# Performance work log

Measured on AMD Instinct MI355X. Metric: run time of the kernel, lower is better.

The kernel has to match this reference:

```python
import jax, jax.numpy as jnp
import numpy as np

B, T, H, W, VD, AD, HD, QD = 256, 10, 7, 7, 512, 128, 256, 128  # QD = 512//latent_dim(4)
BETA = 0.5

def _lin(k, out_d, in_d):
    kw, kb = jax.random.split(k)
    s = 1.0 / np.sqrt(in_d)
    return (jax.random.uniform(kw, (out_d, in_d), jnp.float32, -s, s),
            jax.random.uniform(kb, (out_d,), jnp.float32, -s, s))

def setup_inputs() -> dict:
    key = jax.random.key(0)
    ks = jax.random.split(key, 20)
    d = {}
    d['video'] = jax.random.normal(ks[0], (B, T, H, W, VD), jnp.float32)
    d['audio'] = jax.random.normal(ks[1], (T, B, AD), jnp.float32)
    d['wq'], d['bq'] = _lin(ks[2], QD, VD)
    d['wk'], d['bk'] = _lin(ks[3], QD, VD)
    d['wv'], d['bv'] = _lin(ks[4], VD, VD)
    d['ln_g'] = jnp.ones((VD,), jnp.float32)
    d['ln_b'] = jnp.zeros((VD,), jnp.float32)
    d['w_ave'], d['b_ave'] = _lin(ks[5], HD, VD)
    d['w_v3'], d['b_v3'] = _lin(ks[6], HD, VD)
    d['w_avatt'], d['b_avatt'] = _lin(ks[7], 1, HD)
    d['w_a1'], d['b_a1'] = _lin(ks[8], VD, AD)
    d['w_v1'], d['b_v1'] = _lin(ks[9], VD, VD)
    d['w_bn'], d['b_bn'] = _lin(ks[10], HD, VD)
    d['w_ca'], d['b_ca'] = _lin(ks[11], VD, HD)
    d['w_v2'], d['b_v2'] = _lin(ks[12], HD, VD)
    d['w_a2'], d['b_a2'] = _lin(ks[13], HD, AD)
    d['w_sa'], d['b_sa'] = _lin(ks[14], 1, HD)
    return d

def linear(x, w, b):
    return jnp.matmul(x, w.T) + b

def layer_norm(x, g, b, eps=1e-5):
    mu = jnp.mean(x, -1, keepdims=True)
    var = jnp.mean(jnp.square(x - mu), -1, keepdims=True)
    return (x - mu) * jax.lax.rsqrt(var + eps) * g + b

def reference(video, audio, wq, bq, wk, bk, wv, bv, ln_g, ln_b,
              w_ave, b_ave, w_v3, b_v3, w_avatt, b_avatt,
              w_a1, b_a1, w_v1, b_v1, w_bn, b_bn, w_ca, b_ca,
              w_v2, b_v2, w_a2, b_a2, w_sa, b_sa):
    relu = jax.nn.relu
    audio_bt = jnp.transpose(audio, (1, 0, 2))            # [B,T,AD]
    raw_audio_feature = audio_bt
    audio_feature = audio_bt.reshape(B * T, AD)
    vf = video.reshape(B, T, H * W, VD)                   # [B,T,49,VD]
    raw_visual_feature = vf
    # --- visual self-attention (single head, latent_dim=4) ---
    q = linear(vf, wq, bq).reshape(B * T, H * W, QD)
    k = linear(vf, wk, bk).reshape(B * T, H * W, QD)
    v = linear(vf, wv, bv).reshape(B * T, H * W, VD)
    attn = jax.nn.softmax(jnp.einsum('bnd,bmd->bnm', q, k), axis=-1)
    out = jnp.einsum('bnm,bmd->bnd', attn, v)
    vf2 = layer_norm(vf.reshape(B * T, H * W, VD) + out, ln_g, ln_b)  # dropout in eval mode
    # --- self spatial attention branch ---
    video_avg = relu(linear(vf2.sum(1) / (H * W), w_ave, b_ave))[:, None, :]  # [B*T,1,HD]
    self_q = relu(linear(vf2, w_v3, b_v3)) * video_avg                        # [B*T,49,HD]
    self_maps = jax.nn.softmax(
        jnp.tanh(linear(self_q, w_avatt, b_avatt)).transpose(0, 2, 1), axis=-1)  # [B*T,1,49]
    self_att_feat = jnp.einsum('bon,bnd->bod', self_maps, vf2).reshape(B, T, VD)
    # --- audio-guided channel attention ---
    aq1 = relu(linear(audio_feature, w_a1, b_a1))[:, None, :]                 # [B*T,1,VD]
    vq1 = relu(linear(vf2, w_v1, b_v1))                                       # [B*T,49,VD]
    avq = relu(linear((aq1 * vq1).mean(-2), w_bn, b_bn))                      # [B*T,HD]
    ch_maps = jax.nn.sigmoid(linear(avq, w_ca, b_ca)).reshape(B, T, 1, VD)
    c_att = (raw_visual_feature * (ch_maps + 1.0)).reshape(B * T, H * W, VD)
    # --- audio-guided spatial attention ---
    cq = relu(linear(c_att, w_v2, b_v2))                                      # [B*T,49,HD]
    aq2 = relu(linear(audio_feature, w_a2, b_a2))[:, None, :]                 # [B*T,1,HD]
    sp_maps = jax.nn.softmax(
        jnp.tanh(linear(cq * aq2, w_sa, b_sa)).transpose(0, 2, 1), axis=-1)   # [B*T,1,49]
    c_s = jnp.einsum('bon,bnd->bod', sp_maps, c_att).reshape(B, T, VD)
    c_s = c_s + BETA * jax.nn.sigmoid(self_att_feat) * c_s
    return (c_s, raw_audio_feature)
```

## Files before the change

### kernel.cpp

```cpp
#include <hip/hip_runtime.h>

#define B_   256
#define T_   10
#define BT   2560
#define NSP  49
#define VD   512
#define AD   128
#define HD   256
#define QD   128
#define BETA 0.5f

typedef __bf16 bf16_t;
typedef bf16_t bf16x8 __attribute__((ext_vector_type(8)));
typedef float  f32x4  __attribute__((ext_vector_type(4)));

#define GLDS(g, l) __builtin_amdgcn_global_load_lds(                          \
    (const __attribute__((address_space(1))) void*)(g),                       \
    (__attribute__((address_space(3))) void*)(l), 16, 0, 0)

__global__ __launch_bounds__(128) void k_audio(const float* __restrict__ audio,
                                               float* __restrict__ out2) {
  int bt = blockIdx.x;
  int b = bt / T_, t = bt - b * T_;
  out2[(size_t)bt * AD + threadIdx.x] = audio[((size_t)t * B_ + b) * AD + threadIdx.x];
}

__global__ __launch_bounds__(256) void k_split(const float* __restrict__ x,
                                               bf16_t* __restrict__ hi,
                                               bf16_t* __restrict__ lo) {
  const size_t i8 = (size_t)blockIdx.x * 256 + threadIdx.x;
  const float4 x0 = ((const float4*)x)[2 * i8];
  const float4 x1 = ((const float4*)x)[2 * i8 + 1];
  const float xs[8] = {x0.x, x0.y, x0.z, x0.w, x1.x, x1.y, x1.z, x1.w};
  bf16x8 h, l;
#pragma unroll
  for (int j = 0; j < 8; ++j) {
    const bf16_t hb = (bf16_t)xs[j];
    h[j] = hb;
    l[j] = (bf16_t)(xs[j] - (float)hb);
  }
  ((bf16x8*)hi)[i8] = h;
  ((bf16x8*)lo)[i8] = l;
}

__device__ __forceinline__ bf16x8 ldsread(const unsigned char* plane, int rblk, int lane) {
  const int row = (rblk << 4) + (lane & 15);
  const int chunk = (lane >> 4) ^ ((row >> 1) & 3);
  return *(const bf16x8*)(plane + row * 64 + chunk * 16);
}

template <int ACT>
__global__ __launch_bounds__(256, 2) void k_mgemm(
    const bf16_t* __restrict__ Ahi, const bf16_t* __restrict__ Alo,
    const bf16_t* __restrict__ Whi, const bf16_t* __restrict__ Wlo,
    const float* __restrict__ bias, float* __restrict__ C,
    int M, int N, int K) {
  __shared__ __align__(16) unsigned char smem[2][4][8192];
  const int t = threadIdx.x;
  const int lane = t & 63, wid = t >> 6;
  const int wr = wid >> 1, wc = wid & 1;
  const int rowBase = blockIdx.y * 128;
  const int colBase = blockIdx.x * 128;

  f32x4 acc[4][4] = {};

  const bf16_t* srcs[4] = {Ahi, Alo, Whi, Wlo};
  const int rb[4] = {rowBase, rowBase, colBase, colBase};

  auto stage = [&](int buf, int kt) {
    const int k0 = kt << 5;
#pragma unroll
    for (int p = 0; p < 4; ++p) {
#pragma unroll
      for (int issue = 0; issue < 2; ++issue) {
        const int orow = issue * 64 + wid * 16 + (lane >> 2);
        const int sc = (lane & 3) ^ ((orow >> 1) & 3);
        const bf16_t* g = srcs[p] + (size_t)(rb[p] + orow) * K + k0 + sc * 8;
        unsigned char* l = &smem[buf][p][issue * 4096 + wid * 1024];
        GLDS(g, l);
      }
    }
  };

  const int NK = K >> 5;
  stage(0, 0);
  for (int kt = 0; kt < NK; ++kt) {
    const int cur = kt & 1;
    __syncthreads();
    if (kt + 1 < NK) stage(cur ^ 1, kt + 1);
    const unsigned char* pa_hi = smem[cur][0];
    const unsigned char* pa_lo = smem[cur][1];
    const unsigned char* pw_hi = smem[cur][2];
    const unsigned char* pw_lo = smem[cur][3];
    bf16x8 ah[4], al[4], bh[4], bl[4];
#pragma unroll
    for (int m = 0; m < 4; ++m) {
      ah[m] = ldsread(pa_hi, wr * 4 + m, lane);
      al[m] = ldsread(pa_lo, wr * 4 + m, lane);
    }
#pragma unroll
    for (int n = 0; n < 4; ++n) {
      bh[n] = ldsread(pw_hi, wc * 4 + n, lane);
      bl[n] = ldsread(pw_lo, wc * 4 + n, lane);
    }
#pragma unroll
    for (int m = 0; m < 4; ++m)
#pragma unroll
      for (int n = 0; n < 4; ++n) {
        acc[m][n] = __builtin_amdgcn_mfma_f32_16x16x32_bf16(ah[m], bh[n], acc[m][n], 0, 0, 0);
        acc[m][n] = __builtin_amdgcn_mfma_f32_16x16x32_bf16(ah[m], bl[n], acc[m][n], 0, 0, 0);
        acc[m][n] = __builtin_amdgcn_mfma_f32_16x16x32_bf16(al[m], bh[n], acc[m][n], 0, 0, 0);
      }
  }

  const int r4 = lane >> 4;
  const int cn = lane & 15;
#pragma unroll
  for (int n = 0; n < 4; ++n) {
    const int col = colBase + wc * 64 + n * 16 + cn;
    const float bb = bias[col];
#pragma unroll
    for (int m = 0; m < 4; ++m) {
      const int row0 = rowBase + wr * 64 + m * 16 + r4 * 4;
#pragma unroll
      for (int r = 0; r < 4; ++r) {
        float x = acc[m][n][r] + bb;
        if (ACT == 1) x = fmaxf(x, 0.f);
        C[(size_t)(row0 + r) * N + col] = x;
      }
    }
  }
}

template <int ACT>
__global__ __launch_bounds__(256) void k_gemm(const float* __restrict__ A,
                                              const float* __restrict__ W,
                                              const float* __restrict__ bias,
                                              float* __restrict__ C,
                                              int M, int N, int K, float alpha) {
  __shared__ __align__(16) float As[8][132];
  __shared__ __align__(16) float Ws[8][132];
  const int t = threadIdx.x;
  const int tx = t & 15, ty = t >> 4;
  const int rowBase = blockIdx.y * 128;
  const int colBase = blockIdx.x * 128;
  const int lrow = t >> 1, lq = t & 1;
  const float* Ap = A + (size_t)(rowBase + lrow) * K + lq * 4;
  const float* Wp = W + (size_t)(colBase + lrow) * K + lq * 4;
  float acc[8][8] = {};
  for (int k0 = 0; k0 < K; k0 += 8) {
    const float4 av = *(const float4*)(Ap + k0);
    const float4 wv = *(const float4*)(Wp + k0);
    __syncthreads();
    As[lq * 4 + 0][lrow] = av.x; As[lq * 4 + 1][lrow] = av.y;
    As[lq * 4 + 2][lrow] = av.z; As[lq * 4 + 3][lrow] = av.w;
    Ws[lq * 4 + 0][lrow] = wv.x; Ws[lq * 4 + 1][lrow] = wv.y;
    Ws[lq * 4 + 2][lrow] = wv.z; Ws[lq * 4 + 3][lrow] = wv.w;
    __syncthreads();
#pragma unroll
    for (int kk = 0; kk < 8; ++kk) {
      const float4 a0 = *(const float4*)&As[kk][ty * 8];
      const float4 a1 = *(const float4*)&As[kk][ty * 8 + 4];
      const float4 w0 = *(const float4*)&Ws[kk][tx * 8];
      const float4 w1 = *(const float4*)&Ws[kk][tx * 8 + 4];
      const float a_[8] = {a0.x, a0.y, a0.z, a0.w, a1.x, a1.y, a1.z, a1.w};
      const float w_[8] = {w0.x, w0.y, w0.z, w0.w, w1.x, w1.y, w1.z, w1.w};
#pragma unroll
      for (int i = 0; i < 8; ++i)
#pragma unroll
        for (int j = 0; j < 8; ++j)
          acc[i][j] = fmaf(a_[i], w_[j], acc[i][j]);
    }
  }
  const float4 b0 = *(const float4*)(bias + colBase + tx * 8);
  const float4 b1 = *(const float4*)(bias + colBase + tx * 8 + 4);
  const float bb[8] = {b0.x, b0.y, b0.z, b0.w, b1.x, b1.y, b1.z, b1.w};
#pragma unroll
  for (int i = 0; i < 8; ++i) {
    float* crow = C + (size_t)(rowBase + ty * 8 + i) * N + colBase + tx * 8;
    float o[8];
#pragma unroll
    for (int j = 0; j < 8; ++j) {
      float x = acc[i][j] * alpha + bb[j];
      if (ACT == 1) x = fmaxf(x, 0.f);
      if (ACT == 2) x = 1.f / (1.f + __expf(-x));
      o[j] = x;
    }
    *(float4*)(crow)     = make_float4(o[0], o[1], o[2], o[3]);
    *(float4*)(crow + 4) = make_float4(o[4], o[5], o[6], o[7]);
  }
}

__global__ __launch_bounds__(512) void k_attn(const float* __restrict__ q,
                                              const float* __restrict__ k,
                                              const float* __restrict__ v,
                                              const float* __restrict__ vf,
                                              const float* __restrict__ ln_g,
                                              const float* __restrict__ ln_b,
                                              bf16_t* __restrict__ vf2hi,
                                              bf16_t* __restrict__ vf2lo,
                                              float* __restrict__ vsum) {
  const int bt = blockIdx.x;
  const int t = threadIdx.x;
  __shared__ float qs[NSP][129];
  __shared__ float ks[NSP][129];
  __shared__ float at[NSP][50];
  __shared__ float red[2][NSP][8];
  __shared__ float mu_s[NSP], rs_s[NSP];

  const float* qg = q + (size_t)bt * NSP * QD;
  const float* kg = k + (size_t)bt * NSP * QD;
  for (int i = t; i < NSP * QD; i += 512) {
    int n = i >> 7, c = i & (QD - 1);
    qs[n][c] = qg[i];
    ks[n][c] = kg[i];
  }
  __syncthreads();
  for (int p = t; p < NSP * NSP; p += 512) {
    int n = p / NSP, m = p - n * NSP;
    float s = 0.f;
#pragma unroll 16
    for (int j = 0; j < QD; ++j) s = fmaf(qs[n][j], ks[m][j], s);
    at[n][m] = s;
  }
  __syncthreads();
  if (t < NSP) {
    float mx = -1e30f;
    for (int m2 = 0; m2 < NSP; ++m2) mx = fmaxf(mx, at[t][m2]);
    float sum = 0.f;
    for (int m2 = 0; m2 < NSP; ++m2) { float e = __expf(at[t][m2] - mx); at[t][m2] = e; sum += e; }
    float inv = 1.f / sum;
    for (int m2 = 0; m2 < NSP; ++m2) at[t][m2] *= inv;
  }
  __syncthreads();
  const int d = t;
  const float* vg  = v  + (size_t)bt * NSP * VD + d;
  const float* vfg = vf + (size_t)bt * NSP * VD + d;
  float xv[NSP] = {};
  for (int m2 = 0; m2 < NSP; ++m2) {
    const float vm = vg[(size_t)m2 * VD];
#pragma unroll
    for (int n = 0; n < NSP; ++n) xv[n] = fmaf(at[n][m2], vm, xv[n]);
  }
#pragma unroll
  for (int n = 0; n < NSP; ++n) xv[n] += vfg[(size_t)n * VD];
  const int lane = t & 63, wid = t >> 6;
#pragma unroll
  for (int n = 0; n < NSP; ++n) {
    float s1 = xv[n], s2 = xv[n] * xv[n];
    for (int off = 32; off; off >>= 1) { s1 += __shfl_down(s1, off); s2 += __shfl_down(s2, off); }
    if (lane == 0) { red[0][n][wid] = s1; red[1][n][wid] = s2; }
  }
  __syncthreads();
  if (t < NSP) {
    float s1 = 0.f, s2 = 0.f;
    for (int w2 = 0; w2 < 8; ++w2) { s1 += red[0][t][w2]; s2 += red[1][t][w2]; }
    const float mu = s1 * (1.f / VD);
    const float var = s2 * (1.f / VD) - mu * mu;
    mu_s[t] = mu;
    rs_s[t] = rsqrtf(var + 1e-5f);
  }
  __syncthreads();
  const float gd = ln_g[d], bd = ln_b[d];
  bf16_t* oh = vf2hi + (size_t)bt * NSP * VD + d;
  bf16_t* ol = vf2lo + (size_t)bt * NSP * VD + d;
  float vs = 0.f;
#pragma unroll
  for (int n = 0; n < NSP; ++n) {
    const float y = (xv[n] - mu_s[n]) * rs_s[n] * gd + bd;
    const bf16_t hb = (bf16_t)y;
    oh[(size_t)n * VD] = hb;
    ol[(size_t)n * VD] = (bf16_t)(y - (float)hb);
    vs += y;
  }
  vsum[(size_t)bt * VD + d] = vs;
}

__global__ __launch_bounds__(256) void k_score_einsum(
    const float* __restrict__ Cm, const float* __restrict__ gate,
    const float* __restrict__ wvv, const float* __restrict__ bsc,
    const bf16_t* __restrict__ Vhi, const bf16_t* __restrict__ Vlo,
    const float* __restrict__ saf_in, float* __restrict__ outp) {
  const int bt = blockIdx.x, t = threadIdx.x;
  __shared__ float us[HD];
  __shared__ float sc[NSP];
  __shared__ float mp[NSP + 1];
  us[t] = gate[(size_t)bt * HD + t] * wvv[t];
  __syncthreads();
  const int lane = t & 63, w = t >> 6;
  const float bias0 = bsc[0];
  for (int n = w; n < NSP; n += 4) {
    const float* row = Cm + ((size_t)bt * NSP + n) * HD;
    float s = 0.f;
#pragma unroll
    for (int i = 0; i < HD / 64; ++i) s = fmaf(row[lane + 64 * i], us[lane + 64 * i], s);
    for (int off = 32; off; off >>= 1) s += __shfl_down(s, off);
    if (lane == 0) sc[n] = tanhf(s + bias0);
  }
  __syncthreads();
  if (t == 0) {
    float mx = -1e30f;
    for (int n = 0; n < NSP; ++n) mx = fmaxf(mx, sc[n]);
    float sum = 0.f;
    for (int n = 0; n < NSP; ++n) { float e = __expf(sc[n] - mx); mp[n] = e; sum += e; }
    float inv = 1.f / sum;
    for (int n = 0; n < NSP; ++n) mp[n] *= inv;
  }
  __syncthreads();
  for (int d = t; d < VD; d += 256) {
    const bf16_t* vh = Vhi + (size_t)bt * NSP * VD + d;
    const bf16_t* vl = Vlo + (size_t)bt * NSP * VD + d;
    float a = 0.f;
#pragma unroll
    for (int n = 0; n < NSP; ++n) {
      const float vv = (float)vh[(size_t)n * VD] + (float)vl[(size_t)n * VD];
      a = fmaf(mp[n], vv, a);
    }
    if (saf_in) {
      const float sg = 1.f / (1.f + __expf(-saf_in[(size_t)bt * VD + d]));
      a *= (1.f + BETA * sg);
    }
    outp[(size_t)bt * VD + d] = a;
  }
}

__global__ __launch_bounds__(512) void k_vq1mean(const float* __restrict__ vq1,
                                                 const float* __restrict__ aq1,
                                                 float* __restrict__ tmean) {
  const int bt = blockIdx.x, d = threadIdx.x;
  const float* p = vq1 + (size_t)bt * NSP * VD + d;
  float s = 0.f;
#pragma unroll
  for (int n = 0; n < NSP; ++n) s += p[(size_t)n * VD];
  tmean[(size_t)bt * VD + d] = s * (1.f / 49.f) * aq1[(size_t)bt * VD + d];
}

__global__ __launch_bounds__(256) void k_catt(const float* __restrict__ video,
                                              const float* __restrict__ ch,
                                              bf16_t* __restrict__ hi,
                                              bf16_t* __restrict__ lo) {
  const size_t i8 = (size_t)blockIdx.x * 256 + threadIdx.x;
  const size_t i = i8 * 8;
  const size_t bt = i / ((size_t)NSP * VD);
  const int d = (int)(i & (VD - 1));
  const float4 v0 = ((const float4*)(video + i))[0];
  const float4 v1 = ((const float4*)(video + i))[1];
  const float4 c0 = *(const float4*)(ch + bt * VD + d);
  const float4 c1 = *(const float4*)(ch + bt * VD + d + 4);
  const float xs[8] = {v0.x * (c0.x + 1.f), v0.y * (c0.y + 1.f),
                       v0.z * (c0.z + 1.f), v0.w * (c0.w + 1.f),
                       v1.x * (c1.x + 1.f), v1.y * (c1.y + 1.f),
                       v1.z * (c1.z + 1.f), v1.w * (c1.w + 1.f)};
  bf16x8 h, l;
#pragma unroll
  for (int j = 0; j < 8; ++j) {
    const bf16_t hb = (bf16_t)xs[j];
    h[j] = hb;
    l[j] = (bf16_t)(xs[j] - (float)hb);
  }
  ((bf16x8*)hi)[i8] = h;
  ((bf16x8*)lo)[i8] = l;
}

extern "C" void kernel_launch(void* const* d_in, const int* in_sizes, int n_in,
                              void* d_out, int out_size, void* d_ws, size_t ws_size,
                              hipStream_t stream) {
  const float* video  = (const float*)d_in[0];
  const float* audio  = (const float*)d_in[1];
  const float* wq     = (const float*)d_in[2];  const float* bq     = (const float*)d_in[3];
  const float* wk     = (const float*)d_in[4];  const float* bk     = (const float*)d_in[5];
  const float* wv     = (const float*)d_in[6];  const float* bv     = (const float*)d_in[7];
  const float* ln_g   = (const float*)d_in[8];  const float* ln_b   = (const float*)d_in[9];
  const float* w_ave  = (const float*)d_in[10]; const float* b_ave  = (const float*)d_in[11];
  const float* w_v3   = (const float*)d_in[12]; const float* b_v3   = (const float*)d_in[13];
  const float* w_avatt= (const float*)d_in[14]; const float* b_avatt= (const float*)d_in[15];
  const float* w_a1   = (const float*)d_in[16]; const float* b_a1   = (const float*)d_in[17];
  const float* w_v1   = (const float*)d_in[18]; const float* b_v1   = (const float*)d_in[19];
  const float* w_bn   = (const float*)d_in[20]; const float* b_bn   = (const float*)d_in[21];
  const float* w_ca   = (const float*)d_in[22]; const float* b_ca   = (const float*)d_in[23];
  const float* w_v2   = (const float*)d_in[24]; const float* b_v2   = (const float*)d_in[25];
  const float* w_a2   = (const float*)d_in[26]; const float* b_a2   = (const float*)d_in[27];
  const float* w_sa   = (const float*)d_in[28]; const float* b_sa   = (const float*)d_in[29];

  float* out = (float*)d_out;
  float* out_audio = out + (size_t)BT * VD;

  const size_t M = (size_t)BT * NSP;

  unsigned char* p = (unsigned char*)d_ws;
  auto carve = [&](size_t bytes) { unsigned char* r = p; p += (bytes + 255) & ~(size_t)255; return r; };
  bf16_t* vhi = (bf16_t*)carve(M * VD * 2);
  bf16_t* vlo = (bf16_t*)carve(M * VD * 2);
  bf16_t* wqh = (bf16_t*)carve((size_t)QD * VD * 2);
  bf16_t* wql = (bf16_t*)carve((size_t)QD * VD * 2);
  bf16_t* wkh = (bf16_t*)carve((size_t)QD * VD * 2);
  bf16_t* wkl = (bf16_t*)carve((size_t)QD * VD * 2);
  bf16_t* wvh = (bf16_t*)carve((size_t)VD * VD * 2);
  bf16_t* wvl = (bf16_t*)carve((size_t)VD * VD * 2);
  bf16_t* w3h = (bf16_t*)carve((size_t)HD * VD * 2);
  bf16_t* w3l = (bf16_t*)carve((size_t)HD * VD * 2);
  bf16_t* w1h = (bf16_t*)carve((size_t)VD * VD * 2);
  bf16_t* w1l = (bf16_t*)carve((size_t)VD * VD * 2);
  bf16_t* w2h = (bf16_t*)carve((size_t)HD * VD * 2);
  bf16_t* w2l = (bf16_t*)carve((size_t)HD * VD * 2);
  float* q_   = (float*)carve(M * QD * 4);
  float* k_   = (float*)carve(M * QD * 4);
  float* v_   = (float*)carve(M * VD * 4);
  float* vsum = (float*)carve((size_t)BT * VD * 4);
  float* vavg = (float*)carve((size_t)BT * HD * 4);
  float* aq1  = (float*)carve((size_t)BT * VD * 4);
  float* aq2  = (float*)carve((size_t)BT * HD * 4);
  float* tmean= (float*)carve((size_t)BT * VD * 4);
  float* avq  = (float*)carve((size_t)BT * HD * 4);
  float* saf  = (float*)carve((size_t)BT * VD * 4);
  float* ch   = (float*)carve((size_t)BT * VD * 4);
  float* C1   = q_;
  float* vq1  = v_;
  float* C2   = q_;
  bf16_t *vf2hi = vhi, *vf2lo = vlo, *catthi = vhi, *cattlo = vlo;

  const dim3 blk(256);

  k_audio<<<BT, AD, 0, stream>>>(audio, out_audio);

  k_split<<<(int)(M * VD / 8 / 256), blk, 0, stream>>>(video, vhi, vlo);
  k_split<<<QD * VD / 8 / 256, blk, 0, stream>>>(wq, wqh, wql);
  k_split<<<QD * VD / 8 / 256, blk, 0, stream>>>(wk, wkh, wkl);
  k_split<<<VD * VD / 8 / 256, blk, 0, stream>>>(wv, wvh, wvl);
  k_split<<<HD * VD / 8 / 256, blk, 0, stream>>>(w_v3, w3h, w3l);
  k_split<<<VD * VD / 8 / 256, blk, 0, stream>>>(w_v1, w1h, w1l);
  k_split<<<HD * VD / 8 / 256, blk, 0, stream>>>(w_v2, w2h, w2l);

  k_mgemm<0><<<dim3(QD / 128, M / 128), blk, 0, stream>>>(vhi, vlo, wqh, wql, bq, q_, M, QD, VD);
  k_mgemm<0><<<dim3(QD / 128, M / 128), blk, 0, stream>>>(vhi, vlo, wkh, wkl, bk, k_, M, QD, VD);
  k_mgemm<0><<<dim3(VD / 128, M / 128), blk, 0, stream>>>(vhi, vlo, wvh, wvl, bv, v_, M, VD, VD);
  k_attn<<<BT, 512, 0, stream>>>(q_, k_, v_, video, ln_g, ln_b, vf2hi, vf2lo, vsum);

  k_gemm<1><<<dim3(HD / 128, BT / 128), blk, 0, stream>>>(vsum, w_ave, b_ave, vavg, BT, HD, VD, 1.f / 49.f);
  k_gemm<1><<<dim3(VD / 128, BT / 128), blk, 0, stream>>>(out_audio, w_a1, b_a1, aq1, BT, VD, AD, 1.f);
  k_gemm<1><<<dim3(HD / 128, BT / 128), blk, 0, stream>>>(out_audio, w_a2, b_a2, aq2, BT, HD, AD, 1.f);

  k_mgemm<1><<<dim3(HD / 128, M / 128), blk, 0, stream>>>(vf2hi, vf2lo, w3h, w3l, b_v3, C1, M, HD, VD);
  k_score_einsum<<<BT, 256, 0, stream>>>(C1, vavg, w_avatt, b_avatt, vf2hi, vf2lo, nullptr, saf);

  k_mgemm<1><<<dim3(VD / 128, M / 128), blk, 0, stream>>>(vf2hi, vf2lo, w1h, w1l, b_v1, vq1, M, VD, VD);
  k_vq1mean<<<BT, VD, 0, stream>>>(vq1, aq1, tmean);
  k_gemm<1><<<dim3(HD / 128, BT / 128), blk, 0, stream>>>(tmean, w_bn, b_bn, avq, BT, HD, VD, 1.f);
  k_gemm<2><<<dim3(VD / 128, BT / 128), blk, 0, stream>>>(avq, w_ca, b_ca, ch, BT, VD, HD, 1.f);
  k_catt<<<(int)(M * VD / 8 / 256), blk, 0, stream>>>(video, ch, catthi, cattlo);

  k_mgemm<1><<<dim3(HD / 128, M / 128), blk, 0, stream>>>(catthi, cattlo, w2h, w2l, b_v2, C2, M, HD, VD);
  k_score_einsum<<<BT, 256, 0, stream>>>(C2, aq2, w_sa, b_sa, catthi, cattlo, saf, out);
}
```

Measured before the change: 2.397 ms.

## Fuse QKV projections into one bf16-split GEMM and MFMA-based attention kernel

```diff
diff --git a/kernel.cpp b/kernel.cpp
--- a/kernel.cpp
+++ b/kernel.cpp
@@ -17,12 +17,23 @@
 #define GLDS(g, l) __builtin_amdgcn_global_load_lds(                          \
     (const __attribute__((address_space(1))) void*)(g),                       \
     (__attribute__((address_space(3))) void*)(l), 16, 0, 0)
+#define MFMA16(a, b, c) __builtin_amdgcn_mfma_f32_16x16x32_bf16(a, b, c, 0, 0, 0)
 
 __global__ __launch_bounds__(128) void k_audio(const float* __restrict__ audio,
                                                float* __restrict__ out2) {
   int bt = blockIdx.x;
   int b = bt / T_, t = bt - b * T_;
   out2[(size_t)bt * AD + threadIdx.x] = audio[((size_t)t * B_ + b) * AD + threadIdx.x];
+}
+
+__global__ __launch_bounds__(256) void k_bcat(const float* __restrict__ bq,
+                                              const float* __restrict__ bk,
+                                              const float* __restrict__ bv,
+                                              float* __restrict__ bcat) {
+  int t = blockIdx.x * 256 + threadIdx.x;
+  if (t < 128) bcat[t] = bq[t];
+  else if (t < 256) bcat[t] = bk[t - 128];
+  else if (t < 768) bcat[t] = bv[t - 256];
 }
 
 __global__ __launch_bounds__(256) void k_split(const float* __restrict__ x,
@@ -49,11 +60,12 @@
   return *(const bf16x8*)(plane + row * 64 + chunk * 16);
 }
 
-template <int ACT>
+template <int ACT, int OUT>
 __global__ __launch_bounds__(256, 2) void k_mgemm(
     const bf16_t* __restrict__ Ahi, const bf16_t* __restrict__ Alo,
     const bf16_t* __restrict__ Whi, const bf16_t* __restrict__ Wlo,
     const float* __restrict__ bias, float* __restrict__ C,
+    bf16_t* __restrict__ Chi, bf16_t* __restrict__ Clo,
     int M, int N, int K) {
   __shared__ __align__(16) unsigned char smem[2][4][8192];
   const int t = threadIdx.x;
@@ -107,9 +119,9 @@
     for (int m = 0; m < 4; ++m)
 #pragma unroll
       for (int n = 0; n < 4; ++n) {
-        acc[m][n] = __builtin_amdgcn_mfma_f32_16x16x32_bf16(ah[m], bh[n], acc[m][n], 0, 0, 0);
-        acc[m][n] = __builtin_amdgcn_mfma_f32_16x16x32_bf16(ah[m], bl[n], acc[m][n], 0, 0, 0);
-        acc[m][n] = __builtin_amdgcn_mfma_f32_16x16x32_bf16(al[m], bh[n], acc[m][n], 0, 0, 0);
+        acc[m][n] = MFMA16(ah[m], bh[n], acc[m][n]);
+        acc[m][n] = MFMA16(ah[m], bl[n], acc[m][n]);
+        acc[m][n] = MFMA16(al[m], bh[n], acc[m][n]);
       }
   }
 
@@ -126,9 +138,205 @@
       for (int r = 0; r < 4; ++r) {
         float x = acc[m][n][r] + bb;
         if (ACT == 1) x = fmaxf(x, 0.f);
-        C[(size_t)(row0 + r) * N + col] = x;
-      }
-    }
+        const size_t idx = (size_t)(row0 + r) * N + col;
+        if (OUT == 0) {
+          C[idx] = x;
+        } else {
+          const bf16_t hb = (bf16_t)x;
+          Chi[idx] = hb;
+          Clo[idx] = (bf16_t)(x - (float)hb);
+        }
+      }
+    }
+  }
+}
+
+__global__ __launch_bounds__(512, 4) void k_attn2(
+    const bf16_t* __restrict__ ohi, const bf16_t* __restrict__ olo,
+    const float* __restrict__ vf, const float* __restrict__ ln_g,
+    const float* __restrict__ ln_b, bf16_t* __restrict__ vf2hi,
+    bf16_t* __restrict__ vf2lo, float* __restrict__ vsum) {
+  const int bt = blockIdx.x;
+  const int t = threadIdx.x;
+  const int lane = t & 63, w = t >> 6;
+  const int g = lane >> 4, li = lane & 15;
+  const int r = w & 3, h = w >> 2;
+  const size_t rowbase = (size_t)bt * NSP;
+
+  __shared__ __align__(16) unsigned char smem[69632];
+  __shared__ float red[2][2][4][16];
+  __shared__ float lnred[2][2][4][16];
+  __shared__ float vs_lds[4][512];
+
+  for (int u = t; u < 4096; u += 512) {
+    const int pl = u >> 10, row = (u >> 4) & 63, c = u & 15;
+    const bf16_t* src = (pl & 1) ? olo : ohi;
+    bf16x8 val = *(const bf16x8*)(src + (rowbase + row) * 768 + (pl >> 1) * 128 + c * 8);
+    *(bf16x8*)(smem + pl * 17408 + row * 272 + c * 16) = val;
+  }
+  __syncthreads();
+
+  f32x4 sacc[2] = {};
+#pragma unroll
+  for (int ks = 0; ks < 4; ++ks) {
+    const bf16x8 ah = *(const bf16x8*)(smem + 0 * 17408 + (r * 16 + li) * 272 + ks * 64 + g * 16);
+    const bf16x8 al = *(const bf16x8*)(smem + 1 * 17408 + (r * 16 + li) * 272 + ks * 64 + g * 16);
+#pragma unroll
+    for (int ct = 0; ct < 2; ++ct) {
+      const int m = (h * 2 + ct) * 16 + li;
+      const bf16x8 bh = *(const bf16x8*)(smem + 2 * 17408 + m * 272 + ks * 64 + g * 16);
+      const bf16x8 bl = *(const bf16x8*)(smem + 3 * 17408 + m * 272 + ks * 64 + g * 16);
+      sacc[ct] = MFMA16(ah, bh, sacc[ct]);
+      sacc[ct] = MFMA16(ah, bl, sacc[ct]);
+      sacc[ct] = MFMA16(al, bh, sacc[ct]);
+    }
+  }
+
+  const int m0 = (h * 2 + 0) * 16 + li;
+  const int m1 = (h * 2 + 1) * 16 + li;
+  float e0[4], e1[4];
+#pragma unroll
+  for (int reg = 0; reg < 4; ++reg) {
+    float s0 = (m0 < NSP) ? sacc[0][reg] : -1e30f;
+    float s1 = (m1 < NSP) ? sacc[1][reg] : -1e30f;
+    float mx = fmaxf(s0, s1);
+#pragma unroll
+    for (int off = 1; off < 16; off <<= 1) mx = fmaxf(mx, __shfl_xor(mx, off));
+    if (li == 0) red[0][h][r][g * 4 + reg] = mx;
+  }
+  __syncthreads();
+#pragma unroll
+  for (int reg = 0; reg < 4; ++reg) {
+    const float mx = fmaxf(red[0][0][r][g * 4 + reg], red[0][1][r][g * 4 + reg]);
+    e0[reg] = (m0 < NSP) ? __expf(sacc[0][reg] - mx) : 0.f;
+    e1[reg] = (m1 < NSP) ? __expf(sacc[1][reg] - mx) : 0.f;
+    float su = e0[reg] + e1[reg];
+#pragma unroll
+    for (int off = 1; off < 16; off <<= 1) su += __shfl_xor(su, off);
+    if (li == 0) red[1][h][r][g * 4 + reg] = su;
+  }
+  __syncthreads();
+#pragma unroll
+  for (int reg = 0; reg < 4; ++reg) {
+    const float inv = 1.f / (red[1][0][r][g * 4 + reg] + red[1][1][r][g * 4 + reg]);
+    const int nrow = r * 16 + g * 4 + reg;
+#pragma unroll
+    for (int ct = 0; ct < 2; ++ct) {
+      const int m = (h * 2 + ct) * 16 + li;
+      const float pv = (ct ? e1[reg] : e0[reg]) * inv;
+      const bf16_t ph = (bf16_t)pv;
+      *(bf16_t*)(smem + 0 * 9216 + nrow * 144 + m * 2) = ph;
+      *(bf16_t*)(smem + 1 * 9216 + nrow * 144 + m * 2) = (bf16_t)(pv - (float)ph);
+    }
+  }
+  __syncthreads();
+
+  bf16x8 pa[2][2];
+#pragma unroll
+  for (int ks = 0; ks < 2; ++ks)
+#pragma unroll
+    for (int pl = 0; pl < 2; ++pl)
+      pa[ks][pl] = *(const bf16x8*)(smem + pl * 9216 + (r * 16 + li) * 144 + ks * 64 + g * 16);
+
+  f32x4 oacc[4][4] = {};
+  for (int c = 0; c < 4; ++c) {
+    if (c > 0) __syncthreads();
+    for (int u = t; u < 1024; u += 512) {
+      const int pl = u >> 9, mc = (u >> 6) & 7, dp = u & 63;
+      const bf16_t* src = pl ? olo : ohi;
+      const bf16_t* base = src + (rowbase + mc * 8) * 768 + 256 + c * 128 + dp * 2;
+      bf16x8 r0, r1;
+#pragma unroll
+      for (int j = 0; j < 8; ++j) {
+        const ushort2 vv = *(const ushort2*)(base + (size_t)j * 768);
+        r0[j] = __builtin_bit_cast(bf16_t, (unsigned short)vv.x);
+        r1[j] = __builtin_bit_cast(bf16_t, (unsigned short)vv.y);
+      }
+      unsigned char* vt = smem + 18432 + pl * 18432;
+      *(bf16x8*)(vt + (dp * 2 + 0) * 144 + mc * 16) = r0;
+      *(bf16x8*)(vt + (dp * 2 + 1) * 144 + mc * 16) = r1;
+    }
+    __syncthreads();
+#pragma unroll
+    for (int qd = 0; qd < 4; ++qd) {
+      const int drow = (h * 4 + qd) * 16 + li;
+#pragma unroll
+      for (int ks = 0; ks < 2; ++ks) {
+        const bf16x8 bh = *(const bf16x8*)(smem + 18432 + 0 * 18432 + drow * 144 + ks * 64 + g * 16);
+        const bf16x8 bl = *(const bf16x8*)(smem + 18432 + 1 * 18432 + drow * 144 + ks * 64 + g * 16);
+        oacc[c][qd] = MFMA16(pa[ks][0], bh, oacc[c][qd]);
+        oacc[c][qd] = MFMA16(pa[ks][0], bl, oacc[c][qd]);
+        oacc[c][qd] = MFMA16(pa[ks][1], bh, oacc[c][qd]);
+      }
+    }
+  }
+
+#pragma unroll
+  for (int c = 0; c < 4; ++c)
+#pragma unroll
+    for (int qd = 0; qd < 4; ++qd) {
+      const int d = c * 128 + (h * 4 + qd) * 16 + li;
+#pragma unroll
+      for (int reg = 0; reg < 4; ++reg) {
+        const int n = r * 16 + g * 4 + reg;
+        if (n < NSP) oacc[c][qd][reg] += vf[(rowbase + n) * 512 + d];
+      }
+    }
+  float mu[4], rs[4];
+#pragma unroll
+  for (int reg = 0; reg < 4; ++reg) {
+    float s1 = 0.f, s2 = 0.f;
+#pragma unroll
+    for (int c = 0; c < 4; ++c)
+#pragma unroll
+      for (int qd = 0; qd < 4; ++qd) {
+        const float x = oacc[c][qd][reg];
+        s1 += x; s2 += x * x;
+      }
+#pragma unroll
+    for (int off = 1; off < 16; off <<= 1) {
+      s1 += __shfl_xor(s1, off);
+      s2 += __shfl_xor(s2, off);
+    }
+    if (li == 0) { lnred[0][h][r][g * 4 + reg] = s1; lnred[1][h][r][g * 4 + reg] = s2; }
+  }
+  __syncthreads();
+#pragma unroll
+  for (int reg = 0; reg < 4; ++reg) {
+    const float s1 = lnred[0][0][r][g * 4 + reg] + lnred[0][1][r][g * 4 + reg];
+    const float s2 = lnred[1][0][r][g * 4 + reg] + lnred[1][1][r][g * 4 + reg];
+    const float m_ = s1 * (1.f / VD);
+    mu[reg] = m_;
+    rs[reg] = rsqrtf(s2 * (1.f / VD) - m_ * m_ + 1e-5f);
+  }
+
+#pragma unroll
+  for (int c = 0; c < 4; ++c)
+#pragma unroll
+    for (int qd = 0; qd < 4; ++qd) {
+      const int d = c * 128 + (h * 4 + qd) * 16 + li;
+      const float gd = ln_g[d], bd = ln_b[d];
+      float vp = 0.f;
+#pragma unroll
+      for (int reg = 0; reg < 4; ++reg) {
+        const int n = r * 16 + g * 4 + reg;
+        const float y = (oacc[c][qd][reg] - mu[reg]) * rs[reg] * gd + bd;
+        if (n < NSP) {
+          const size_t idx = (rowbase + n) * 512 + d;
+          const bf16_t hb = (bf16_t)y;
+          vf2hi[idx] = hb;
+          vf2lo[idx] = (bf16_t)(y - (float)hb);
+          vp += y;
+        }
+      }
+#pragma unroll
+      for (int off = 16; off < 64; off <<= 1) vp += __shfl_xor(vp, off);
+      if (g == 0) vs_lds[r][d] = vp;
+    }
+  __syncthreads();
+  if (t < 512) {
+    const float s = vs_lds[0][t] + vs_lds[1][t] + vs_lds[2][t] + vs_lds[3][t];
+    vsum[(size_t)bt * 512 + t] = s;
   }
 }
 
@@ -191,91 +399,6 @@
   }
 }
 
-__global__ __launch_bounds__(512) void k_attn(const float* __restrict__ q,
-                                              const float* __restrict__ k,
-                                              const float* __restrict__ v,
-                                              const float* __restrict__ vf,
-                                              const float* __restrict__ ln_g,
-                                              const float* __restrict__ ln_b,
-                                              bf16_t* __restrict__ vf2hi,
-                                              bf16_t* __restrict__ vf2lo,
-                                              float* __restrict__ vsum) {
-  const int bt = blockIdx.x;
-  const int t = threadIdx.x;
-  __shared__ float qs[NSP][129];
-  __shared__ float ks[NSP][129];
-  __shared__ float at[NSP][50];
-  __shared__ float red[2][NSP][8];
-  __shared__ float mu_s[NSP], rs_s[NSP];
-
-  const float* qg = q + (size_t)bt * NSP * QD;
-  const float* kg = k + (size_t)bt * NSP * QD;
-  for (int i = t; i < NSP * QD; i += 512) {
-    int n = i >> 7, c = i & (QD - 1);
-    qs[n][c] = qg[i];
-    ks[n][c] = kg[i];
-  }
-  __syncthreads();
-  for (int p = t; p < NSP * NSP; p += 512) {
-    int n = p / NSP, m = p - n * NSP;
-    float s = 0.f;
-#pragma unroll 16
-    for (int j = 0; j < QD; ++j) s = fmaf(qs[n][j], ks[m][j], s);
-    at[n][m] = s;
-  }
-  __syncthreads();
-  if (t < NSP) {
-    float mx = -1e30f;
-    for (int m2 = 0; m2 < NSP; ++m2) mx = fmaxf(mx, at[t][m2]);
-    float sum = 0.f;
-    for (int m2 = 0; m2 < NSP; ++m2) { float e = __expf(at[t][m2] - mx); at[t][m2] = e; sum += e; }
-    float inv = 1.f / sum;
-    for (int m2 = 0; m2 < NSP; ++m2) at[t][m2] *= inv;
-  }
-  __syncthreads();
-  const int d = t;
-  const float* vg  = v  + (size_t)bt * NSP * VD + d;
-  const float* vfg = vf + (size_t)bt * NSP * VD + d;
-  float xv[NSP] = {};
-  for (int m2 = 0; m2 < NSP; ++m2) {
-    const float vm = vg[(size_t)m2 * VD];
-#pragma unroll
-    for (int n = 0; n < NSP; ++n) xv[n] = fmaf(at[n][m2], vm, xv[n]);
-  }
-#pragma unroll
-  for (int n = 0; n < NSP; ++n) xv[n] += vfg[(size_t)n * VD];
-  const int lane = t & 63, wid = t >> 6;
-#pragma unroll
-  for (int n = 0; n < NSP; ++n) {
-    float s1 = xv[n], s2 = xv[n] * xv[n];
-    for (int off = 32; off; off >>= 1) { s1 += __shfl_down(s1, off); s2 += __shfl_down(s2, off); }
-    if (lane == 0) { red[0][n][wid] = s1; red[1][n][wid] = s2; }
-  }
-  __syncthreads();
-  if (t < NSP) {
-    float s1 = 0.f, s2 = 0.f;
-    for (int w2 = 0; w2 < 8; ++w2) { s1 += red[0][t][w2]; s2 += red[1][t][w2]; }
-    const float mu = s1 * (1.f / VD);
-    const float var = s2 * (1.f / VD) - mu * mu;
-    mu_s[t] = mu;
-    rs_s[t] = rsqrtf(var + 1e-5f);
-  }
-  __syncthreads();
-  const float gd = ln_g[d], bd = ln_b[d];
-  bf16_t* oh = vf2hi + (size_t)bt * NSP * VD + d;
-  bf16_t* ol = vf2lo + (size_t)bt * NSP * VD + d;
-  float vs = 0.f;
-#pragma unroll
-  for (int n = 0; n < NSP; ++n) {
-    const float y = (xv[n] - mu_s[n]) * rs_s[n] * gd + bd;
-    const bf16_t hb = (bf16_t)y;
-    oh[(size_t)n * VD] = hb;
-    ol[(size_t)n * VD] = (bf16_t)(y - (float)hb);
-    vs += y;
-  }
-  vsum[(size_t)bt * VD + d] = vs;
-}
-
 __global__ __launch_bounds__(256) void k_score_einsum(
     const float* __restrict__ Cm, const float* __restrict__ gate,
     const float* __restrict__ wvv, const float* __restrict__ bsc,
@@ -386,69 +509,70 @@
   float* out_audio = out + (size_t)BT * VD;
 
   const size_t M = (size_t)BT * NSP;
+  const size_t Mpad = M + 64;
 
   unsigned char* p = (unsigned char*)d_ws;
   auto carve = [&](size_t bytes) { unsigned char* r = p; p += (bytes + 255) & ~(size_t)255; return r; };
-  bf16_t* vhi = (bf16_t*)carve(M * VD * 2);
-  bf16_t* vlo = (bf16_t*)carve(M * VD * 2);
-  bf16_t* wqh = (bf16_t*)carve((size_t)QD * VD * 2);
-  bf16_t* wql = (bf16_t*)carve((size_t)QD * VD * 2);
-  bf16_t* wkh = (bf16_t*)carve((size_t)QD * VD * 2);
-  bf16_t* wkl = (bf16_t*)carve((size_t)QD * VD * 2);
-  bf16_t* wvh = (bf16_t*)carve((size_t)VD * VD * 2);
-  bf16_t* wvl = (bf16_t*)carve((size_t)VD * VD * 2);
-  bf16_t* w3h = (bf16_t*)carve((size_t)HD * VD * 2);
-  bf16_t* w3l = (bf16_t*)carve((size_t)HD * VD * 2);
-  bf16_t* w1h = (bf16_t*)carve((size_t)VD * VD * 2);
-  bf16_t* w1l = (bf16_t*)carve((size_t)VD * VD * 2);
-  bf16_t* w2h = (bf16_t*)carve((size_t)HD * VD * 2);
-  bf16_t* w2l = (bf16_t*)carve((size_t)HD * VD * 2);
-  float* q_   = (float*)carve(M * QD * 4);
-  float* k_   = (float*)carve(M * QD * 4);
-  float* v_   = (float*)carve(M * VD * 4);
-  float* vsum = (float*)carve((size_t)BT * VD * 4);
-  float* vavg = (float*)carve((size_t)BT * HD * 4);
-  float* aq1  = (float*)carve((size_t)BT * VD * 4);
-  float* aq2  = (float*)carve((size_t)BT * HD * 4);
-  float* tmean= (float*)carve((size_t)BT * VD * 4);
-  float* avq  = (float*)carve((size_t)BT * HD * 4);
-  float* saf  = (float*)carve((size_t)BT * VD * 4);
-  float* ch   = (float*)carve((size_t)BT * VD * 4);
-  float* C1   = q_;
-  float* vq1  = v_;
-  float* C2   = q_;
-  bf16_t *vf2hi = vhi, *vf2lo = vlo, *catthi = vhi, *cattlo = vlo;
+  bf16_t* vhi  = (bf16_t*)carve(M * VD * 2);
+  bf16_t* vlo  = (bf16_t*)carve(M * VD * 2);
+  bf16_t* wch  = (bf16_t*)carve((size_t)768 * VD * 2);
+  bf16_t* wcl  = (bf16_t*)carve((size_t)768 * VD * 2);
+  bf16_t* w3h  = (bf16_t*)carve((size_t)HD * VD * 2);
+  bf16_t* w3l  = (bf16_t*)carve((size_t)HD * VD * 2);
+  bf16_t* w1h  = (bf16_t*)carve((size_t)VD * VD * 2);
+  bf16_t* w1l  = (bf16_t*)carve((size_t)VD * VD * 2);
+  bf16_t* w2h  = (bf16_t*)carve((size_t)HD * VD * 2);
+  bf16_t* w2l  = (bf16_t*)carve((size_t)HD * VD * 2);
+  float*  bcat = (float*)carve(768 * 4);
+  bf16_t* o_hi = (bf16_t*)carve(Mpad * 768 * 2 * 2);
+  bf16_t* o_lo = o_hi + Mpad * 768;
+  float* vsum  = (float*)carve((size_t)BT * VD * 4);
+  float* vavg  = (float*)carve((size_t)BT * HD * 4);
+  float* aq1   = (float*)carve((size_t)BT * VD * 4);
+  float* aq2   = (float*)carve((size_t)BT * HD * 4);
+  float* tmean = (float*)carve((size_t)BT * VD * 4);
+  float* avq   = (float*)carve((size_t)BT * HD * 4);
+  float* saf   = (float*)carve((size_t)BT * VD * 4);
+  float* ch    = (float*)carve((size_t)BT * VD * 4);
+  float*  vq1    = (float*)o_hi;
+  bf16_t* catthi = o_hi;
+  bf16_t* cattlo = o_hi + M * VD;
+  float*  C12    = (float*)(o_hi + 2 * M * VD);
+  bf16_t *vf2hi = vhi, *vf2lo = vlo;
 
   const dim3 blk(256);
 
   k_audio<<<BT, AD, 0, stream>>>(audio, out_audio);
 
   k_split<<<(int)(M * VD / 8 / 256), blk, 0, stream>>>(video, vhi, vlo);
-  k_split<<<QD * VD / 8 / 256, blk, 0, stream>>>(wq, wqh, wql);
-  k_split<<<QD * VD / 8 / 256, blk, 0, stream>>>(wk, wkh, wkl);
-  k_split<<<VD * VD / 8 / 256, blk, 0, stream>>>(wv, wvh, wvl);
+  k_split<<<QD * VD / 8 / 256, blk, 0, stream>>>(wq, wch, wcl);
+  k_split<<<QD * VD / 8 / 256, blk, 0, stream>>>(wk, wch + (size_t)QD * VD, wcl + (size_t)QD * VD);
+  k_split<<<VD * VD / 8 / 256, blk, 0, stream>>>(wv, wch + (size_t)2 * QD * VD, wcl + (size_t)2 * QD * VD);
   k_split<<<HD * VD / 8 / 256, blk, 0, stream>>>(w_v3, w3h, w3l);
   k_split<<<VD * VD / 8 / 256, blk, 0, stream>>>(w_v1, w1h, w1l);
   k_split<<<HD * VD / 8 / 256, blk, 0, stream>>>(w_v2, w2h, w2l);
-
-  k_mgemm<0><<<dim3(QD / 128, M / 128), blk, 0, stream>>>(vhi, vlo, wqh, wql, bq, q_, M, QD, VD);
-  k_mgemm<0><<<dim3(QD / 128, M / 128), blk, 0, stream>>>(vhi, vlo, wkh, wkl, bk, k_, M, QD, VD);
-  k_mgemm<0><<<dim3(VD / 128, M / 128), blk, 0, stream>>>(vhi, vlo, wvh, wvl, bv, v_, M, VD, VD);
-  k_attn<<<BT, 512, 0, stream>>>(q_, k_, v_, video, ln_g, ln_b, vf2hi, vf2lo, vsum);
+  k_bcat<<<3, blk, 0, stream>>>(bq, bk, bv, bcat);
+
+  k_mgemm<0, 1><<<dim3(6, M / 128), blk, 0, stream>>>(vhi, vlo, wch, wcl, bcat,
+                                                      nullptr, o_hi, o_lo, M, 768, VD);
+  k_attn2<<<BT, 512, 0, stream>>>(o_hi, o_lo, video, ln_g, ln_b, vf2hi, vf2lo, vsum);
 
   k_gemm<1><<<dim3(HD / 128, BT / 128), blk, 0, stream>>>(vsum, w_ave, b_ave, vavg, BT, HD, VD, 1.f / 49.f);
   k_gemm<1><<<dim3(VD / 128, BT / 128), blk, 0, stream>>>(out_audio, w_a1, b_a1, aq1, BT, VD, AD, 1.f);
   k_gemm<1><<<dim3(HD / 128, BT / 128), blk, 0, stream>>>(out_audio, w_a2, b_a2, aq2, BT, HD, AD, 1.f);
 
-  k_mgemm<1><<<dim3(HD / 128, M / 128), blk, 0, stream>>>(vf2hi, vf2lo, w3h, w3l, b_v3, C1, M, HD, VD);
-  k_score_einsum<<<BT, 256, 0, stream>>>(C1, vavg, w_avatt, b_avatt, vf2hi, vf2lo, nullptr, saf);
-
-  k_mgemm<1><<<dim3(VD / 128, M / 128), blk, 0, stream>>>(vf2hi, vf2lo, w1h, w1l, b_v1, vq1, M, VD, VD);
+  k_mgemm<1, 0><<<dim3(HD / 128, M / 128), blk, 0, stream>>>(vf2hi, vf2lo, w3h, w3l, b_v3,
+                                                             C12, nullptr, nullptr, M, HD, VD);
+  k_score_einsum<<<BT, 256, 0, stream>>>(C12, vavg, w_avatt, b_avatt, vf2hi, vf2lo, nullptr, saf);
+
+  k_mgemm<1, 0><<<dim3(VD / 128, M / 128), blk, 0, stream>>>(vf2hi, vf2lo, w1h, w1l, b_v1,
+                                                             vq1, nullptr, nullptr, M, VD, VD);
   k_vq1mean<<<BT, VD, 0, stream>>>(vq1, aq1, tmean);
   k_gemm<1><<<dim3(HD / 128, BT / 128), blk, 0, stream>>>(tmean, w_bn, b_bn, avq, BT, HD, VD, 1.f);
   k_gemm<2><<<dim3(VD / 128, BT / 128), blk, 0, stream>>>(avq, w_ca, b_ca, ch, BT, VD, HD, 1.f);
   k_catt<<<(int)(M * VD / 8 / 256), blk, 0, stream>>>(video, ch, catthi, cattlo);
 
-  k_mgemm<1><<<dim3(HD / 128, M / 128), blk, 0, stream>>>(catthi, cattlo, w2h, w2l, b_v2, C2, M, HD, VD);
-  k_score_einsum<<<BT, 256, 0, stream>>>(C2, aq2, w_sa, b_sa, catthi, cattlo, saf, out);
-}
+  k_mgemm<1, 0><<<dim3(HD / 128, M / 128), blk, 0, stream>>>(catthi, cattlo, w2h, w2l, b_v2,
+                                                             C12, nullptr, nullptr, M, HD, VD);
+  k_score_einsum<<<BT, 256, 0, stream>>>(C12, aq2, w_sa, b_sa, catthi, cattlo, saf, out);
+}
```

Result: faster. 2.214 ms (-7.6%).
